# Kernel optimization log

Measured on AMD Instinct MI355X. Metric: run time of the kernel, lower is better.

The kernel has to match this reference:

```python
import jax, jax.numpy as jnp
import numpy as np
import math

B, S, E, H, F = 2, 2048, 1024, 16, 4096
D = E // H
EPS = 1e-5


def _layernorm(x, g, b):
    mu = jnp.mean(x, axis=-1, keepdims=True)
    var = jnp.mean(jnp.square(x - mu), axis=-1, keepdims=True)
    return (x - mu) * jax.lax.rsqrt(var + EPS) * g + b


def _xavier(k, fan_in, fan_out):
    limit = math.sqrt(6.0 / (fan_in + fan_out))
    return jax.random.uniform(k, (fan_in, fan_out), jnp.float32, -limit, limit)


def setup_inputs() -> dict:
    key = jax.random.key(0)
    ks = jax.random.split(key, 8)
    x = jax.random.normal(ks[0], (B, S, E), jnp.float32)
    # causal mask: 1 where attendable, 0 where masked (masked_fill at mask==0)
    mask = jnp.tril(jnp.ones((S, S), jnp.int32))[None, None]  # [1,1,S,S]
    return {
        "x": x,
        "mask": mask,
        "Wq": _xavier(ks[1], E, E), "bq": jnp.zeros((E,), jnp.float32),
        "Wk": _xavier(ks[2], E, E), "bk": jnp.zeros((E,), jnp.float32),
        "Wv": _xavier(ks[3], E, E), "bv": jnp.zeros((E,), jnp.float32),
        "Wo": _xavier(ks[4], E, E), "bo": jnp.zeros((E,), jnp.float32),
        "W1": _xavier(ks[5], E, F), "b1": jnp.zeros((F,), jnp.float32),
        "W2": _xavier(ks[6], F, E), "b2": jnp.zeros((E,), jnp.float32),
        "ln1_g": jnp.ones((E,), jnp.float32), "ln1_b": jnp.zeros((E,), jnp.float32),
        "ln2_g": jnp.ones((E,), jnp.float32), "ln2_b": jnp.zeros((E,), jnp.float32),
    }


def reference(x, mask, Wq, bq, Wk, bk, Wv, bv, Wo, bo, W1, b1, W2, b2,
              ln1_g, ln1_b, ln2_g, ln2_b):
    n = _layernorm(x, ln1_g, ln1_b)
    # project and split heads: [B,S,E] -> [B,H,S,D]
    def heads(w, b):
        return (n @ w + b).reshape(B, S, H, D).transpose(0, 2, 1, 3)
    Q, K, V = heads(Wq, bq), heads(Wk, bk), heads(Wv, bv)
    scores = jnp.einsum('bhsd,bhtd->bhst', Q, K) / math.sqrt(D)  # [B,H,S,S]
    scores = jnp.where(mask == 0, jnp.float32(-1e9), scores)
    attn = jax.nn.softmax(scores, axis=-1)
    ctx = jnp.einsum('bhst,bhtd->bhsd', attn, V)
    ctx = ctx.transpose(0, 2, 1, 3).reshape(B, S, E)
    attn_out = ctx @ Wo + bo
    x = _layernorm(x + attn_out, ln2_g, ln2_b)
    ffn = jax.nn.gelu(x @ W1 + b1, approximate=False) @ W2 + b2
    return x + ffn
```

## Files before the change

### kernel.cpp

```cpp
#include <hip/hip_runtime.h>
#include <cmath>

typedef unsigned short u16;
typedef unsigned int u32;
typedef __bf16 bf16x8 __attribute__((ext_vector_type(8)));
typedef float f32x4 __attribute__((ext_vector_type(4)));

#define SEQ 2048
#define EMB 1024
#define NHEAD 16
#define HDIM 64
#define FFDIM 4096
#define NBATCH 2
#define QKVLD 3072
#define PWS 68

#define QSCALE 0.18033688011112042f

__device__ __forceinline__ u16 f2bf(float f) {
  u32 u = __float_as_uint(f);
  u32 r = u + 0x7fffu + ((u >> 16) & 1u);
  return (u16)(r >> 16);
}

__device__ __forceinline__ float ex2(float x) {
#if __has_builtin(__builtin_amdgcn_exp2f)
  return __builtin_amdgcn_exp2f(x);
#else
  return exp2f(x);
#endif
}

__device__ __forceinline__ float geluf(float x) {
  float u = 0.7978845608028654f * (x + 0.044715f * x * x * x);
  float e = ex2(2.8853900817779268f * u);
  return x - x / (e + 1.0f);
}

__device__ __forceinline__ void gload16(const void* g, void* l) {
  __builtin_amdgcn_global_load_lds(
      (const __attribute__((address_space(1))) unsigned int*)g,
      (__attribute__((address_space(3))) unsigned int*)l, 16, 0, 0);
}

__global__ __launch_bounds__(256)
void wtrans_kernel(const float* __restrict__ W, u16* __restrict__ WT, int K, int N) {
  __shared__ float tile[32][33];
  int tx = threadIdx.x & 31, ty = threadIdx.x >> 5;
  int n0 = blockIdx.x * 32, k0 = blockIdx.y * 32;
#pragma unroll
  for (int i = 0; i < 32; i += 8)
    tile[ty + i][tx] = W[(size_t)(k0 + ty + i) * N + (n0 + tx)];
  __syncthreads();
#pragma unroll
  for (int i = 0; i < 32; i += 8)
    WT[(size_t)(n0 + ty + i) * K + (k0 + tx)] = f2bf(tile[tx][ty + i]);
}

__global__ __launch_bounds__(256)
void wtrans4_kernel(const float* __restrict__ W0, const float* __restrict__ W1_,
                    const float* __restrict__ W2_, const float* __restrict__ W3,
                    u16* __restrict__ Dqkv, u16* __restrict__ Do) {
  __shared__ float tile[32][33];
  int z = blockIdx.z;
  const float* W = (z == 0) ? W0 : (z == 1) ? W1_ : (z == 2) ? W2_ : W3;
  u16* D = (z < 3) ? (Dqkv + (size_t)z * EMB * EMB) : Do;
  int tx = threadIdx.x & 31, ty = threadIdx.x >> 5;
  int n0 = blockIdx.x * 32, k0 = blockIdx.y * 32;
#pragma unroll
  for (int i = 0; i < 32; i += 8)
    tile[ty + i][tx] = W[(size_t)(k0 + ty + i) * EMB + (n0 + tx)];
  __syncthreads();
#pragma unroll
  for (int i = 0; i < 32; i += 8)
    D[(size_t)(n0 + ty + i) * EMB + (k0 + tx)] = f2bf(tile[tx][ty + i]);
}

__global__ __launch_bounds__(256)
void vtrans_kernel(const u16* __restrict__ QKV, u16* __restrict__ Vt) {
  __shared__ u16 tile[64 * 72];
  int bh = blockIdx.y, b = bh >> 4, h = bh & 15;
  int s0 = blockIdx.x * 64;
  const u16* src = QKV + (size_t)b * SEQ * QKVLD + 2048 + (size_t)h * HDIM;
  int tid = threadIdx.x;
#pragma unroll
  for (int cc = 0; cc < 2; ++cc) {
    int c = tid + cc * 256;
    int s = c >> 3, d0 = (c & 7) * 8;
    uint4 v = *(const uint4*)(src + (size_t)(s0 + s) * QKVLD + d0);
    *(uint4*)(&tile[s * 72 + d0]) = v;
  }
  __syncthreads();
  u16* dst = Vt + (size_t)bh * HDIM * SEQ;
#pragma unroll
  for (int cc = 0; cc < 2; ++cc) {
    int c = tid + cc * 256;
    int d = c >> 3, t0l = (c & 7) * 8;
    union { uint4 u; u16 s[8]; } ou;
#pragma unroll
    for (int j = 0; j < 8; ++j) ou.s[j] = tile[(t0l + j) * 72 + d];
    *(uint4*)(dst + (size_t)d * SEQ + s0 + t0l) = ou.u;
  }
}

__global__ __launch_bounds__(256)
void ln_kernel(const float* __restrict__ in, const float* __restrict__ gamma,
               const float* __restrict__ beta, u16* __restrict__ outb) {
  int w = threadIdx.x >> 6, lane = threadIdx.x & 63;
  int row = blockIdx.x * 4 + w;
  size_t base = (size_t)row * EMB;
  float4 v[4];
  float s = 0.f, q = 0.f;
#pragma unroll
  for (int j = 0; j < 4; ++j) {
    v[j] = *(const float4*)(in + base + j * 256 + lane * 4);
    s += v[j].x + v[j].y + v[j].z + v[j].w;
    q += v[j].x * v[j].x + v[j].y * v[j].y + v[j].z * v[j].z + v[j].w * v[j].w;
  }
#pragma unroll
  for (int off = 1; off < 64; off <<= 1) {
    s += __shfl_xor(s, off);
    q += __shfl_xor(q, off);
  }
  float mean = s * (1.0f / EMB);
  float var = q * (1.0f / EMB) - mean * mean;
  float rstd = rsqrtf(var + 1e-5f);
#pragma unroll
  for (int j = 0; j < 4; ++j) {
    int c = j * 256 + lane * 4;
    float4 g4 = *(const float4*)(gamma + c);
    float4 b4 = *(const float4*)(beta + c);
    ushort4 ob;
    ob.x = f2bf((v[j].x - mean) * rstd * g4.x + b4.x);
    ob.y = f2bf((v[j].y - mean) * rstd * g4.y + b4.y);
    ob.z = f2bf((v[j].z - mean) * rstd * g4.z + b4.z);
    ob.w = f2bf((v[j].w - mean) * rstd * g4.w + b4.w);
    *(ushort4*)(outb + base + c) = ob;
  }
}

__global__ __launch_bounds__(256)
void ln2f_kernel(const float* __restrict__ p, size_t pstride,
                 const float* __restrict__ bias, const float* __restrict__ resid,
                 const float* __restrict__ gamma, const float* __restrict__ beta,
                 u16* __restrict__ outb, float* __restrict__ outf) {
  int w = threadIdx.x >> 6, lane = threadIdx.x & 63;
  int row = blockIdx.x * 4 + w;
  size_t base = (size_t)row * EMB;
  float4 v[4];
  float s = 0.f, q = 0.f;
#pragma unroll
  for (int j = 0; j < 4; ++j) {
    int c = j * 256 + lane * 4;
    float4 a = *(const float4*)(p + base + c);
    float4 b = *(const float4*)(p + pstride + base + c);
    float4 r = *(const float4*)(resid + base + c);
    float4 bb = *(const float4*)(bias + c);
    v[j].x = a.x + b.x + r.x + bb.x;
    v[j].y = a.y + b.y + r.y + bb.y;
    v[j].z = a.z + b.z + r.z + bb.z;
    v[j].w = a.w + b.w + r.w + bb.w;
    s += v[j].x + v[j].y + v[j].z + v[j].w;
    q += v[j].x * v[j].x + v[j].y * v[j].y + v[j].z * v[j].z + v[j].w * v[j].w;
  }
#pragma unroll
  for (int off = 1; off < 64; off <<= 1) {
    s += __shfl_xor(s, off);
    q += __shfl_xor(q, off);
  }
  float mean = s * (1.0f / EMB);
  float var = q * (1.0f / EMB) - mean * mean;
  float rstd = rsqrtf(var + 1e-5f);
#pragma unroll
  for (int j = 0; j < 4; ++j) {
    int c = j * 256 + lane * 4;
    float4 g4 = *(const float4*)(gamma + c);
    float4 b4 = *(const float4*)(beta + c);
    float y0 = (v[j].x - mean) * rstd * g4.x + b4.x;
    float y1 = (v[j].y - mean) * rstd * g4.y + b4.y;
    float y2 = (v[j].z - mean) * rstd * g4.z + b4.z;
    float y3 = (v[j].w - mean) * rstd * g4.w + b4.w;
    ushort4 ob;
    ob.x = f2bf(y0); ob.y = f2bf(y1); ob.z = f2bf(y2); ob.w = f2bf(y3);
    *(ushort4*)(outb + base + c) = ob;
    *(float4*)(outf + base + c) = make_float4(y0, y1, y2, y3);
  }
}

__global__ __launch_bounds__(256)
void reduce2_kernel(const float* __restrict__ p, size_t pstride,
                    const float* __restrict__ bias, const float* __restrict__ resid,
                    float* __restrict__ out, int ncols) {
  size_t i = ((size_t)blockIdx.x * 256 + threadIdx.x) * 4;
  float4 a = *(const float4*)(p + i);
  float4 b = *(const float4*)(p + pstride + i);
  float4 r = *(const float4*)(resid + i);
  int col = (int)(i & (size_t)(ncols - 1));
  float4 bb = *(const float4*)(bias + col);
  float4 o;
  o.x = a.x + b.x + r.x + bb.x;
  o.y = a.y + b.y + r.y + bb.y;
  o.z = a.z + b.z + r.z + bb.z;
  o.w = a.w + b.w + r.w + bb.w;
  *(float4*)(out + i) = o;
}

__global__ __launch_bounds__(256)
void gemm_bt(const u16* __restrict__ A, const u16* __restrict__ BT,
             const float* __restrict__ bias, const float* __restrict__ bias2,
             const float* __restrict__ bias3, void* __restrict__ out,
             const float* __restrict__ resid, int M, int N, int K,
             int mode, float scale, int ksplit,
             float* __restrict__ partial, size_t pstride) {
  __shared__ __align__(16) u16 As[128 * 64];
  __shared__ __align__(16) u16 Bs[128 * 64];
  int tid = threadIdx.x;
  int lane = tid & 63, w = tid >> 6;
  int wm = w >> 1, wn = w & 1;
  int g = lane >> 4, lr = lane & 15;
  int m0 = blockIdx.y * 128, n0 = blockIdx.x * 128;
  int z = blockIdx.z;
  int kbeg = z * ksplit, kend = kbeg + ksplit;

  f32x4 acc[4][4];
#pragma unroll
  for (int mt = 0; mt < 4; ++mt)
#pragma unroll
    for (int nt = 0; nt < 4; ++nt) {
      acc[mt][nt][0] = 0.f; acc[mt][nt][1] = 0.f;
      acc[mt][nt][2] = 0.f; acc[mt][nt][3] = 0.f;
    }

  size_t ao[4], bo_[4];
  int lo[4];
#pragma unroll
  for (int cc = 0; cc < 4; ++cc) {
    int c = tid + cc * 256;
    int row = c >> 3, slot = c & 7;
    int gc = slot ^ (row & 7);
    ao[cc] = (size_t)(m0 + row) * K + gc * 8;
    bo_[cc] = (size_t)(n0 + row) * K + gc * 8;
    lo[cc] = c * 8;
  }
  int swz[2];
#pragma unroll
  for (int kk = 0; kk < 2; ++kk) swz[kk] = ((kk * 4 + g) ^ (lr & 7)) * 8;

  for (int k0 = kbeg; k0 < kend; k0 += 64) {
    __syncthreads();
#pragma unroll
    for (int cc = 0; cc < 4; ++cc) gload16(A + ao[cc] + k0, As + lo[cc]);
#pragma unroll
    for (int cc = 0; cc < 4; ++cc) gload16(BT + bo_[cc] + k0, Bs + lo[cc]);
    __syncthreads();
#pragma unroll
    for (int kk = 0; kk < 2; ++kk) {
      bf16x8 af[4], bfr[4];
#pragma unroll
      for (int mt = 0; mt < 4; ++mt)
        af[mt] = *(const bf16x8*)(As + (wm * 64 + mt * 16 + lr) * 64 + swz[kk]);
#pragma unroll
      for (int nt = 0; nt < 4; ++nt)
        bfr[nt] = *(const bf16x8*)(Bs + (wn * 64 + nt * 16 + lr) * 64 + swz[kk]);
#pragma unroll
      for (int mt = 0; mt < 4; ++mt)
#pragma unroll
        for (int nt = 0; nt < 4; ++nt)
          acc[mt][nt] = __builtin_amdgcn_mfma_f32_16x16x32_bf16(af[mt], bfr[nt], acc[mt][nt], 0, 0, 0);
    }
  }

  float* pz = partial + (size_t)z * pstride;
#pragma unroll
  for (int mt = 0; mt < 4; ++mt) {
    int row = m0 + wm * 64 + mt * 16 + g * 4;
#pragma unroll
    for (int nt = 0; nt < 4; ++nt) {
      int col = n0 + wn * 64 + nt * 16 + lr;
      float bcol;
      if (mode == 3) {
        int which = col >> 10;
        const float* bp = (which == 0) ? bias : (which == 1) ? bias2 : bias3;
        bcol = bp[col & 1023];
      } else if (mode != 4) {
        bcol = bias[col];
      } else {
        bcol = 0.f;
      }
#pragma unroll
      for (int r = 0; r < 4; ++r) {
        float vacc = acc[mt][nt][r] + bcol;
        size_t idx = (size_t)(row + r) * N + col;
        if (mode == 0)      ((u16*)out)[idx] = f2bf(vacc * scale);
        else if (mode == 1) ((u16*)out)[idx] = f2bf(geluf(vacc));
        else if (mode == 2) ((float*)out)[idx] = vacc + resid[idx];
        else if (mode == 3) ((u16*)out)[idx] = f2bf(col < 1024 ? vacc * QSCALE : vacc);
        else                pz[idx] = vacc;
      }
    }
  }
}

__shared__ __align__(16) u16 attn_Kt[64 * 64];
__shared__ __align__(16) u16 attn_VT[64 * 64];
__shared__ __align__(16) u16 attn_Pw[2][4][16 * PWS];

template <int S0>
__device__ __forceinline__ void attn_tile(
    int t0, const int* q0, int w, int g, int lr, const bf16x8& ones,
    bf16x8 (&qf)[2][2], f32x4 (&lacc)[2], f32x4 (&oacc)[2][4]) {
  f32x4 sacc[2][4];
#pragma unroll
  for (int s = S0; s < 2; ++s)
#pragma unroll
    for (int nt = 0; nt < 4; ++nt) {
      sacc[s][nt][0] = 0.f; sacc[s][nt][1] = 0.f;
      sacc[s][nt][2] = 0.f; sacc[s][nt][3] = 0.f;
    }
#pragma unroll
  for (int kk = 0; kk < 2; ++kk)
#pragma unroll
    for (int nt = 0; nt < 4; ++nt) {
      int sw = ((kk * 4 + g) ^ lr) & 7;
      bf16x8 bfr = *(const bf16x8*)(&attn_Kt[(nt * 16 + lr) * 64 + sw * 8]);
      if (S0 == 0)
        sacc[0][nt] = __builtin_amdgcn_mfma_f32_16x16x32_bf16(qf[0][kk], bfr, sacc[0][nt], 0, 0, 0);
      sacc[1][nt] = __builtin_amdgcn_mfma_f32_16x16x32_bf16(qf[1][kk], bfr, sacc[1][nt], 0, 0, 0);
    }

#pragma unroll
  for (int s = S0; s < 2; ++s) {
    bool diag = (t0 == q0[s]);
#pragma unroll
    for (int r = 0; r < 4; ++r) {
#pragma unroll
      for (int nt = 0; nt < 4; ++nt) {
        float pv = ex2(sacc[s][nt][r]);
        if (diag && (nt * 16 + lr > w * 16 + g * 4 + r)) pv = 0.f;
        attn_Pw[s][w][(g * 4 + r) * PWS + nt * 16 + lr] = f2bf(pv);
      }
    }
  }

#pragma unroll
  for (int kk = 0; kk < 2; ++kk) {
    bf16x8 pf0, pf1;
    if (S0 == 0) pf0 = *(const bf16x8*)(&attn_Pw[0][w][lr * PWS + kk * 32 + g * 8]);
    pf1 = *(const bf16x8*)(&attn_Pw[1][w][lr * PWS + kk * 32 + g * 8]);
#pragma unroll
    for (int nt = 0; nt < 4; ++nt) {
      int sw = ((kk * 4 + g) ^ lr) & 7;
      bf16x8 vf = *(const bf16x8*)(&attn_VT[(nt * 16 + lr) * 64 + sw * 8]);
      if (S0 == 0)
        oacc[0][nt] = __builtin_amdgcn_mfma_f32_16x16x32_bf16(pf0, vf, oacc[0][nt], 0, 0, 0);
      oacc[1][nt] = __builtin_amdgcn_mfma_f32_16x16x32_bf16(pf1, vf, oacc[1][nt], 0, 0, 0);
    }
    if (S0 == 0)
      lacc[0] = __builtin_amdgcn_mfma_f32_16x16x32_bf16(pf0, ones, lacc[0], 0, 0, 0);
    lacc[1] = __builtin_amdgcn_mfma_f32_16x16x32_bf16(pf1, ones, lacc[1], 0, 0, 0);
  }
}

__global__ __launch_bounds__(256)
void attn2_kernel(const u16* __restrict__ QKV, const u16* __restrict__ Vt,
                  u16* __restrict__ ctx) {
  int tid = threadIdx.x, lane = tid & 63, w = tid >> 6;
  int g = lane >> 4, lr = lane & 15;
  int bh = blockIdx.y, b = bh >> 4, h = bh & 15;
  int q0[2];
  q0[0] = blockIdx.x * 64;
  q0[1] = (SEQ / 64 - 1 - blockIdx.x) * 64;
  const u16* Qh = QKV + (size_t)b * SEQ * QKVLD + (size_t)h * HDIM;
  const u16* Kh = Qh + 1024;
  const u16* Vth = Vt + (size_t)bh * HDIM * SEQ;

  bf16x8 ones;
#pragma unroll
  for (int j = 0; j < 8; ++j) ones[j] = (__bf16)1.0f;

  bf16x8 qf[2][2];
#pragma unroll
  for (int s = 0; s < 2; ++s)
#pragma unroll
    for (int kk = 0; kk < 2; ++kk)
      qf[s][kk] = *(const bf16x8*)(Qh + (size_t)(q0[s] + w * 16 + lr) * QKVLD + kk * 32 + g * 8);

  f32x4 lacc[2];
  f32x4 oacc[2][4];
#pragma unroll
  for (int s = 0; s < 2; ++s) {
    lacc[s][0] = 0.f; lacc[s][1] = 0.f; lacc[s][2] = 0.f; lacc[s][3] = 0.f;
#pragma unroll
    for (int nt = 0; nt < 4; ++nt) {
      oacc[s][nt][0] = 0.f; oacc[s][nt][1] = 0.f;
      oacc[s][nt][2] = 0.f; oacc[s][nt][3] = 0.f;
    }
  }

  int c1 = tid, c2 = tid + 256;
  int t1 = c1 >> 3, ch1 = (c1 ^ t1) & 7;
  int t2 = c2 >> 3, ch2 = (c2 ^ t2) & 7;
  for (int t0 = 0; t0 <= q0[1]; t0 += 64) {
    __syncthreads();
    gload16(Kh + (size_t)(t0 + t1) * QKVLD + ch1 * 8, attn_Kt + c1 * 8);
    gload16(Kh + (size_t)(t0 + t2) * QKVLD + ch2 * 8, attn_Kt + c2 * 8);
    gload16(Vth + (size_t)t1 * SEQ + t0 + ch1 * 8, attn_VT + c1 * 8);
    gload16(Vth + (size_t)t2 * SEQ + t0 + ch2 * 8, attn_VT + c2 * 8);
    __syncthreads();

    if (t0 <= q0[0])
      attn_tile<0>(t0, q0, w, g, lr, ones, qf, lacc, oacc);
    else
      attn_tile<1>(t0, q0, w, g, lr, ones, qf, lacc, oacc);
  }

#pragma unroll
  for (int s = 0; s < 2; ++s) {
    int srow = q0[s] + w * 16 + g * 4;
    float inv[4];
#pragma unroll
    for (int r = 0; r < 4; ++r) inv[r] = 1.0f / lacc[s][r];
#pragma unroll
    for (int nt = 0; nt < 4; ++nt) {
      int col = h * HDIM + nt * 16 + lr;
#pragma unroll
      for (int r = 0; r < 4; ++r) {
        float o = oacc[s][nt][r] * inv[r];
        ctx[((size_t)b * SEQ + srow + r) * EMB + col] = f2bf(o);
      }
    }
  }
}

extern "C" void kernel_launch(void* const* d_in, const int* in_sizes, int n_in,
                              void* d_out, int out_size, void* d_ws, size_t ws_size,
                              hipStream_t stream) {
  const float* x    = (const float*)d_in[0];
  const float* Wq   = (const float*)d_in[2];
  const float* bq   = (const float*)d_in[3];
  const float* Wk   = (const float*)d_in[4];
  const float* bk   = (const float*)d_in[5];
  const float* Wv   = (const float*)d_in[6];
  const float* bv   = (const float*)d_in[7];
  const float* Wo   = (const float*)d_in[8];
  const float* bo   = (const float*)d_in[9];
  const float* W1   = (const float*)d_in[10];
  const float* b1   = (const float*)d_in[11];
  const float* W2   = (const float*)d_in[12];
  const float* b2   = (const float*)d_in[13];
  const float* ln1g = (const float*)d_in[14];
  const float* ln1b = (const float*)d_in[15];
  const float* ln2g = (const float*)d_in[16];
  const float* ln2b = (const float*)d_in[17];

  char* ws = (char*)d_ws;
  u16* WqkvT = (u16*)(ws + ((size_t)0 << 20));
  u16* WoT   = (u16*)(ws + ((size_t)6 << 20));
  u16* W1T   = (u16*)(ws + ((size_t)8 << 20));
  u16* W2T   = (u16*)(ws + ((size_t)16 << 20));
  u16* xb    = (u16*)(ws + ((size_t)24 << 20));
  u16* QKVb  = (u16*)(ws + ((size_t)32 << 20));
  u16* ctxb  = (u16*)(ws + ((size_t)56 << 20));
  float* x2f = (float*)(ws + ((size_t)48 << 20));
  u16* x2b   = xb;
  u16* VtG   = (u16*)(ws + ((size_t)64 << 20));
  float* pWo = (float*)(ws + ((size_t)64 << 20));
  u16* h1    = (u16*)(ws + ((size_t)64 << 20));
  float* pF2 = (float*)(ws + ((size_t)0 << 20));

  dim3 blk(256);
  const int M = NBATCH * SEQ;

  wtrans4_kernel<<<dim3(32, 32, 4), blk, 0, stream>>>(Wq, Wk, Wv, Wo, WqkvT, WoT);
  wtrans_kernel<<<dim3(128, 32), blk, 0, stream>>>(W1, W1T, EMB, FFDIM);
  wtrans_kernel<<<dim3(32, 128), blk, 0, stream>>>(W2, W2T, FFDIM, EMB);

  ln_kernel<<<M / 4, blk, 0, stream>>>(x, ln1g, ln1b, xb);

  gemm_bt<<<dim3(QKVLD / 128, M / 128), blk, 0, stream>>>(
      xb, WqkvT, bq, bk, bv, QKVb, nullptr, M, QKVLD, EMB, 3, 1.0f, EMB, nullptr, 0);

  vtrans_kernel<<<dim3(SEQ / 64, NBATCH * NHEAD), blk, 0, stream>>>(QKVb, VtG);

  attn2_kernel<<<dim3(SEQ / 128, NBATCH * NHEAD), blk, 0, stream>>>(QKVb, VtG, ctxb);

  gemm_bt<<<dim3(EMB / 128, M / 128, 2), blk, 0, stream>>>(
      ctxb, WoT, nullptr, nullptr, nullptr, nullptr, nullptr, M, EMB, EMB, 4, 1.0f,
      EMB / 2, pWo, (size_t)4 << 20);

  ln2f_kernel<<<M / 4, blk, 0, stream>>>(pWo, (size_t)4 << 20, bo, x, ln2g, ln2b,
                                         x2b, x2f);

  gemm_bt<<<dim3(FFDIM / 128, M / 128), blk, 0, stream>>>(
      x2b, W1T, b1, nullptr, nullptr, h1, nullptr, M, FFDIM, EMB, 1, 1.0f, EMB, nullptr, 0);

  gemm_bt<<<dim3(EMB / 128, M / 128, 2), blk, 0, stream>>>(
      h1, W2T, nullptr, nullptr, nullptr, nullptr, nullptr, M, EMB, FFDIM, 4, 1.0f,
      FFDIM / 2, pF2, (size_t)8 << 20);
  reduce2_kernel<<<M * EMB / 1024, blk, 0, stream>>>(pF2, (size_t)8 << 20, b2, x2f,
                                                     (float*)d_out, EMB);
}
```

Measured before the change: 418.8 us.

## Replace GEMM with 8-wave double-buffered pipelined kernel and larger tiles

Replaces the simple single-buffered 128x128 GEMM with a templated 512-thread kernel that uses 256-wide N tiles and BM of 128 or 256. Global-to-LDS loads for later k-steps are interleaved with the MFMA phases across four LDS buffers, using explicit s_barrier, vmcnt waits and setprio. The intent is to hide memory latency and raise MFMA utilisation. The cost is much more LDS per block, fewer blocks on the smaller GEMMs, and fragile hand-written wait counts.

```diff
diff --git a/kernel.cpp b/kernel.cpp
--- a/kernel.cpp
+++ b/kernel.cpp
@@ -205,75 +205,141 @@
   *(float4*)(out + i) = o;
 }
 
-__global__ __launch_bounds__(256)
-void gemm_bt(const u16* __restrict__ A, const u16* __restrict__ BT,
-             const float* __restrict__ bias, const float* __restrict__ bias2,
-             const float* __restrict__ bias3, void* __restrict__ out,
-             const float* __restrict__ resid, int M, int N, int K,
-             int mode, float scale, int ksplit,
-             float* __restrict__ partial, size_t pstride) {
-  __shared__ __align__(16) u16 As[128 * 64];
-  __shared__ __align__(16) u16 Bs[128 * 64];
+
+#define BARM asm volatile("s_barrier" ::: "memory")
+#define VMWS asm volatile("s_waitcnt vmcnt(%0)" ::"n"(4 + RA) : "memory")
+#define VMW0 asm volatile("s_waitcnt vmcnt(0)" ::: "memory")
+#define NOSTG ((void)0)
+#define NOWT ((void)0)
+
+#define STG_A(t, d, kh)                                                       \
+  { _Pragma("unroll")                                                         \
+    for (int j = 0; j < RA; ++j)                                              \
+      gload16(A + (size_t)sgA[j] + kbeg + (t) * 64 + (kh) * 32,               \
+              As + ((d) * 2 + (kh)) * ABUF + slA[j]); }
+
+#define STG_B(t, d, kh)                                                       \
+  { _Pragma("unroll")                                                         \
+    for (int j = 0; j < 2; ++j)                                               \
+      gload16(BT + (size_t)sgB[j] + kbeg + (t) * 64 + (kh) * 32,              \
+              Bs + ((d) * 2 + (kh)) * 8192 + slB[j]); }
+
+#define PHASE(d, kk, mh, STAGE, WAITC)                                        \
+  {                                                                           \
+    if ((mh) == 0) {                                                          \
+      _Pragma("unroll")                                                       \
+      for (int nt = 0; nt < 4; ++nt)                                          \
+        bfr[nt] = *(const bf16x8*)(Bs + ((d) * 2 + (kk)) * 8192 + boff +      \
+                                   nt * 512);                                 \
+    }                                                                         \
+    bf16x8 af[MT2];                                                           \
+    _Pragma("unroll")                                                         \
+    for (int mi = 0; mi < MT2; ++mi)                                          \
+      af[mi] = *(const bf16x8*)(As + ((d) * 2 + (kk)) * ABUF + aoff +         \
+                                ((mh) * MT2 + mi) * 512);                     \
+    STAGE;                                                                    \
+    BARM;                                                                     \
+    __builtin_amdgcn_sched_barrier(0);                                        \
+    __builtin_amdgcn_s_setprio(1);                                            \
+    _Pragma("unroll")                                                         \
+    for (int mi = 0; mi < MT2; ++mi)                                          \
+      _Pragma("unroll")                                                       \
+      for (int nt = 0; nt < 4; ++nt)                                          \
+        acc[(mh) * MT2 + mi][nt] = __builtin_amdgcn_mfma_f32_16x16x32_bf16(   \
+            af[mi], bfr[nt], acc[(mh) * MT2 + mi][nt], 0, 0, 0);              \
+    __builtin_amdgcn_s_setprio(0);                                            \
+    __builtin_amdgcn_sched_barrier(0);                                        \
+    WAITC;                                                                    \
+    BARM;                                                                     \
+  }
+
+template <int BM>
+__global__ __launch_bounds__(512, 2)
+void gemm8(const u16* __restrict__ A, const u16* __restrict__ BT,
+           const float* __restrict__ bias, const float* __restrict__ bias2,
+           const float* __restrict__ bias3, void* __restrict__ out,
+           const float* __restrict__ resid, int M, int N, int K,
+           int mode, float scale, int ksplit,
+           float* __restrict__ partial, size_t pstride) {
+  constexpr int MT = BM / 32;
+  constexpr int MT2 = MT / 2;
+  constexpr int RA = BM / 128;
+  constexpr int ABUF = BM * 32;
+  __shared__ __align__(16) u16 As[4 * ABUF];
+  __shared__ __align__(16) u16 Bs[4 * 8192];
+
   int tid = threadIdx.x;
   int lane = tid & 63, w = tid >> 6;
-  int wm = w >> 1, wn = w & 1;
+  int wm = w >> 2, wn = w & 3;
   int g = lane >> 4, lr = lane & 15;
-  int m0 = blockIdx.y * 128, n0 = blockIdx.x * 128;
+  int m0 = blockIdx.y * BM, n0 = blockIdx.x * 256;
   int z = blockIdx.z;
-  int kbeg = z * ksplit, kend = kbeg + ksplit;
-
-  f32x4 acc[4][4];
-#pragma unroll
-  for (int mt = 0; mt < 4; ++mt)
+  size_t kbeg = (size_t)z * ksplit;
+  int nk = ksplit >> 6, npair = nk >> 1;
+
+  int phys = ((lr & 1) * 4 + g) ^ ((lr >> 1) & 7);
+  int aoff = wm * (BM / 2) * 32 + (lr >> 1) * 64 + phys * 8;
+  int boff = wn * 2048 + (lr >> 1) * 64 + phys * 8;
+
+  int sgA[RA], slA[RA];
+#pragma unroll
+  for (int j = 0; j < RA; ++j) {
+    int c = tid + j * 512;
+    int sr = c >> 3, ph = c & 7, l = ph ^ (sr & 7);
+    sgA[j] = (m0 + 2 * sr + (l >> 2)) * K + (l & 3) * 8;
+    slA[j] = c * 8;
+  }
+  int sgB[2], slB[2];
+#pragma unroll
+  for (int j = 0; j < 2; ++j) {
+    int c = tid + j * 512;
+    int sr = c >> 3, ph = c & 7, l = ph ^ (sr & 7);
+    sgB[j] = (n0 + 2 * sr + (l >> 2)) * K + (l & 3) * 8;
+    slB[j] = c * 8;
+  }
+
+  f32x4 acc[MT][4];
+#pragma unroll
+  for (int mt = 0; mt < MT; ++mt)
 #pragma unroll
     for (int nt = 0; nt < 4; ++nt) {
       acc[mt][nt][0] = 0.f; acc[mt][nt][1] = 0.f;
       acc[mt][nt][2] = 0.f; acc[mt][nt][3] = 0.f;
     }
 
-  size_t ao[4], bo_[4];
-  int lo[4];
-#pragma unroll
-  for (int cc = 0; cc < 4; ++cc) {
-    int c = tid + cc * 256;
-    int row = c >> 3, slot = c & 7;
-    int gc = slot ^ (row & 7);
-    ao[cc] = (size_t)(m0 + row) * K + gc * 8;
-    bo_[cc] = (size_t)(n0 + row) * K + gc * 8;
-    lo[cc] = c * 8;
-  }
-  int swz[2];
-#pragma unroll
-  for (int kk = 0; kk < 2; ++kk) swz[kk] = ((kk * 4 + g) ^ (lr & 7)) * 8;
-
-  for (int k0 = kbeg; k0 < kend; k0 += 64) {
-    __syncthreads();
-#pragma unroll
-    for (int cc = 0; cc < 4; ++cc) gload16(A + ao[cc] + k0, As + lo[cc]);
-#pragma unroll
-    for (int cc = 0; cc < 4; ++cc) gload16(BT + bo_[cc] + k0, Bs + lo[cc]);
-    __syncthreads();
-#pragma unroll
-    for (int kk = 0; kk < 2; ++kk) {
-      bf16x8 af[4], bfr[4];
-#pragma unroll
-      for (int mt = 0; mt < 4; ++mt)
-        af[mt] = *(const bf16x8*)(As + (wm * 64 + mt * 16 + lr) * 64 + swz[kk]);
-#pragma unroll
-      for (int nt = 0; nt < 4; ++nt)
-        bfr[nt] = *(const bf16x8*)(Bs + (wn * 64 + nt * 16 + lr) * 64 + swz[kk]);
-#pragma unroll
-      for (int mt = 0; mt < 4; ++mt)
-#pragma unroll
-        for (int nt = 0; nt < 4; ++nt)
-          acc[mt][nt] = __builtin_amdgcn_mfma_f32_16x16x32_bf16(af[mt], bfr[nt], acc[mt][nt], 0, 0, 0);
-    }
+  bf16x8 bfr[4];
+
+  STG_B(0, 0, 0); STG_A(0, 0, 0); STG_B(0, 0, 1); STG_A(0, 0, 1);
+  STG_B(1, 1, 0); STG_A(1, 1, 0); STG_B(1, 1, 1);
+  VMWS; BARM;
+
+  for (int it = 0; it < npair - 1; ++it) {
+    int t1 = 2 * it + 1, t2 = 2 * it + 2, t3 = 2 * it + 3;
+    PHASE(0, 0, 0, STG_A(t1, 1, 1), NOWT)
+    PHASE(0, 0, 1, STG_B(t2, 0, 0), NOWT)
+    PHASE(0, 1, 0, STG_A(t2, 0, 0), NOWT)
+    PHASE(0, 1, 1, STG_B(t2, 0, 1), VMWS)
+    PHASE(1, 0, 0, STG_A(t2, 0, 1), NOWT)
+    PHASE(1, 0, 1, STG_B(t3, 1, 0), NOWT)
+    PHASE(1, 1, 0, STG_A(t3, 1, 0), NOWT)
+    PHASE(1, 1, 1, STG_B(t3, 1, 1), VMWS)
+  }
+  {
+    int t1 = nk - 1;
+    PHASE(0, 0, 0, STG_A(t1, 1, 1), NOWT)
+    PHASE(0, 0, 1, NOSTG, NOWT)
+    PHASE(0, 1, 0, NOSTG, NOWT)
+    PHASE(0, 1, 1, NOSTG, VMW0)
+    PHASE(1, 0, 0, NOSTG, NOWT)
+    PHASE(1, 0, 1, NOSTG, NOWT)
+    PHASE(1, 1, 0, NOSTG, NOWT)
+    PHASE(1, 1, 1, NOSTG, NOWT)
   }
 
   float* pz = partial + (size_t)z * pstride;
 #pragma unroll
-  for (int mt = 0; mt < 4; ++mt) {
-    int row = m0 + wm * 64 + mt * 16 + g * 4;
+  for (int mt = 0; mt < MT; ++mt) {
+    int row = m0 + wm * (BM / 2) + mt * 16 + g * 4;
 #pragma unroll
     for (int nt = 0; nt < 4; ++nt) {
       int col = n0 + wn * 64 + nt * 16 + lr;
@@ -469,6 +535,7 @@
   float* pF2 = (float*)(ws + ((size_t)0 << 20));
 
   dim3 blk(256);
+  dim3 blk512(512);
   const int M = NBATCH * SEQ;
 
   wtrans4_kernel<<<dim3(32, 32, 4), blk, 0, stream>>>(Wq, Wk, Wv, Wo, WqkvT, WoT);
@@ -477,24 +544,25 @@
 
   ln_kernel<<<M / 4, blk, 0, stream>>>(x, ln1g, ln1b, xb);
 
-  gemm_bt<<<dim3(QKVLD / 128, M / 128), blk, 0, stream>>>(
+  gemm8<256><<<dim3(QKVLD / 256, M / 256), blk512, 0, stream>>>(
       xb, WqkvT, bq, bk, bv, QKVb, nullptr, M, QKVLD, EMB, 3, 1.0f, EMB, nullptr, 0);
 
   vtrans_kernel<<<dim3(SEQ / 64, NBATCH * NHEAD), blk, 0, stream>>>(QKVb, VtG);
 
   attn2_kernel<<<dim3(SEQ / 128, NBATCH * NHEAD), blk, 0, stream>>>(QKVb, VtG, ctxb);
 
-  gemm_bt<<<dim3(EMB / 128, M / 128, 2), blk, 0, stream>>>(
+  gemm8<128><<<dim3(EMB / 256, M / 128, 2), blk512, 0, stream>>>(
       ctxb, WoT, nullptr, nullptr, nullptr, nullptr, nullptr, M, EMB, EMB, 4, 1.0f,
       EMB / 2, pWo, (size_t)4 << 20);
 
   ln2f_kernel<<<M / 4, blk, 0, stream>>>(pWo, (size_t)4 << 20, bo, x, ln2g, ln2b,
                                          x2b, x2f);
 
-  gemm_bt<<<dim3(FFDIM / 128, M / 128), blk, 0, stream>>>(
-      x2b, W1T, b1, nullptr, nullptr, h1, nullptr, M, FFDIM, EMB, 1, 1.0f, EMB, nullptr, 0);
-
-  gemm_bt<<<dim3(EMB / 128, M / 128, 2), blk, 0, stream>>>(
+  gemm8<256><<<dim3(FFDIM / 256, M / 256), blk512, 0, stream>>>(
+      x2b, W1T, b1, nullptr, nullptr, h1, nullptr, M, FFDIM, EMB, 1, 1.0f, EMB,
+      nullptr, 0);
+
+  gemm8<128><<<dim3(EMB / 256, M / 128, 2), blk512, 0, stream>>>(
       h1, W2T, nullptr, nullptr, nullptr, nullptr, nullptr, M, EMB, FFDIM, 4, 1.0f,
       FFDIM / 2, pF2, (size_t)8 << 20);
   reduce2_kernel<<<M * EMB / 1024, blk, 0, stream>>>(pF2, (size_t)8 << 20, b2, x2f,
```

Result: slower. 428.8 us (+2.4%).

## Add software-pipelined double-buffered GEMM with XCD tile swizzle for Wo and FFN

Applied to the files above, without the earlier changes.

Adds a new GEMM kernel, gemm8n, used for the Wo projection and both FFN GEMMs. It double-buffers K-halves in LDS, interleaves async global-to-LDS loads with MFMA phases, uses swizzled inline ds_read_b128 addressing, raises wave priority during MFMA and allows two blocks per CU. It also remaps block indices so each XCD works on a spatially clustered group of tiles, aiming for better L2 reuse, and applies a simpler XCD swizzle to the existing gemm_bt. The cost targeted is load latency and barrier stalls in the GEMMs. In exchange the code is complex, relies on hand-placed waitcnts and assumes the grid size divides evenly by 8.

```diff
diff --git a/kernel.cpp b/kernel.cpp
--- a/kernel.cpp
+++ b/kernel.cpp
@@ -41,6 +41,40 @@
   __builtin_amdgcn_global_load_lds(
       (const __attribute__((address_space(1))) unsigned int*)g,
       (__attribute__((address_space(3))) unsigned int*)l, 16, 0, 0);
+}
+
+__device__ __forceinline__ u32 lds_addr(const void* p) {
+  return (u32)(size_t)(const __attribute__((address_space(3))) void*)p;
+}
+
+template <int IMM>
+__device__ __forceinline__ bf16x8 dsr16(u32 a) {
+  bf16x8 r;
+  asm volatile("ds_read_b128 %0, %1 offset:%2" : "=v"(r) : "v"(a), "n"(IMM));
+  return r;
+}
+
+__device__ __forceinline__ void xcd_swizzle(int gx, int gy, int& bx, int& by) {
+  int nwg = gx * gy;
+  int lin = blockIdx.x + gx * blockIdx.y;
+  int q = nwg >> 3;
+  int nl = (lin & 7) * q + (lin >> 3);
+  bx = nl % gx;
+  by = nl / gx;
+}
+
+template <int TX>
+__device__ __forceinline__ void xcd_tile_swizzle(int gx, int gy, int& bx, int& by) {
+  int nwg = gx * gy;
+  int lin = blockIdx.x + gx * blockIdx.y;
+  int c = lin & 7;
+  int wdx = lin >> 3;
+  int q = nwg >> 3;
+  int TY = q / TX;
+  int ncx = gx / TX;
+  int xt = c % ncx, yt = c / ncx;
+  bx = xt * TX + wdx % TX;
+  by = yt * TY + wdx / TX;
 }
 
 __global__ __launch_bounds__(256)
@@ -218,7 +252,9 @@
   int lane = tid & 63, w = tid >> 6;
   int wm = w >> 1, wn = w & 1;
   int g = lane >> 4, lr = lane & 15;
-  int m0 = blockIdx.y * 128, n0 = blockIdx.x * 128;
+  int bx, by;
+  xcd_swizzle(gridDim.x, gridDim.y, bx, by);
+  int m0 = by * 128, n0 = bx * 128;
   int z = blockIdx.z;
   int kbeg = z * ksplit, kend = kbeg + ksplit;
 
@@ -268,6 +304,161 @@
         for (int nt = 0; nt < 4; ++nt)
           acc[mt][nt] = __builtin_amdgcn_mfma_f32_16x16x32_bf16(af[mt], bfr[nt], acc[mt][nt], 0, 0, 0);
     }
+  }
+
+  float* pz = partial + (size_t)z * pstride;
+#pragma unroll
+  for (int mt = 0; mt < 4; ++mt) {
+    int row = m0 + wm * 64 + mt * 16 + g * 4;
+#pragma unroll
+    for (int nt = 0; nt < 4; ++nt) {
+      int col = n0 + wn * 64 + nt * 16 + lr;
+      float bcol;
+      if (mode == 3) {
+        int which = col >> 10;
+        const float* bp = (which == 0) ? bias : (which == 1) ? bias2 : bias3;
+        bcol = bp[col & 1023];
+      } else if (mode != 4) {
+        bcol = bias[col];
+      } else {
+        bcol = 0.f;
+      }
+#pragma unroll
+      for (int r = 0; r < 4; ++r) {
+        float vacc = acc[mt][nt][r] + bcol;
+        size_t idx = (size_t)(row + r) * N + col;
+        if (mode == 0)      ((u16*)out)[idx] = f2bf(vacc * scale);
+        else if (mode == 1) ((u16*)out)[idx] = f2bf(geluf(vacc));
+        else if (mode == 2) ((float*)out)[idx] = vacc + resid[idx];
+        else if (mode == 3) ((u16*)out)[idx] = f2bf(col < 1024 ? vacc * QSCALE : vacc);
+        else                pz[idx] = vacc;
+      }
+    }
+  }
+}
+
+
+#define BARM __builtin_amdgcn_s_barrier()
+#define VMW6 asm volatile("s_waitcnt vmcnt(6)")
+#define VMW0 asm volatile("s_waitcnt vmcnt(0)")
+#define NOSTG ((void)0)
+#define NOWT ((void)0)
+#define NABUF (128 * 32)
+
+#define STGN_A(t, d, kh)                                                      \
+  { gload16(A + (size_t)sgA[0] + kbeg + (t) * 64 + (kh) * 32,                 \
+            As + ((d) * 2 + (kh)) * NABUF + sl[0]);                           \
+    gload16(A + (size_t)sgA[1] + kbeg + (t) * 64 + (kh) * 32,                 \
+            As + ((d) * 2 + (kh)) * NABUF + sl[1]); }
+
+#define STGN_B(t, d, kh)                                                      \
+  { gload16(BT + (size_t)sgB[0] + kbeg + (t) * 64 + (kh) * 32,                \
+            Bs + ((d) * 2 + (kh)) * NABUF + sl[0]);                           \
+    gload16(BT + (size_t)sgB[1] + kbeg + (t) * 64 + (kh) * 32,                \
+            Bs + ((d) * 2 + (kh)) * NABUF + sl[1]); }
+
+#define PHASEN(d, kk, mh, STAGE, WAITC)                                       \
+  {                                                                           \
+    const u32 bA = bB + ((d) * 2 + (kk)) * (NABUF * 2);                       \
+    const u32 aA = aB + ((d) * 2 + (kk)) * (NABUF * 2);                       \
+    if ((mh) == 0) {                                                          \
+      bfr[0] = dsr16<0>(bA);                                                  \
+      bfr[1] = dsr16<1024>(bA);                                               \
+      bfr[2] = dsr16<2048>(bA);                                               \
+      bfr[3] = dsr16<3072>(bA);                                               \
+    }                                                                         \
+    bf16x8 af[2];                                                             \
+    af[0] = dsr16<(((mh) * 2 + 0) * 1024)>(aA);                               \
+    af[1] = dsr16<(((mh) * 2 + 1) * 1024)>(aA);                               \
+    STAGE;                                                                    \
+    BARM;                                                                     \
+    asm volatile("s_waitcnt lgkmcnt(0)");                                     \
+    __builtin_amdgcn_sched_barrier(0);                                        \
+    __builtin_amdgcn_s_setprio(1);                                            \
+    _Pragma("unroll")                                                         \
+    for (int mi = 0; mi < 2; ++mi)                                            \
+      _Pragma("unroll")                                                       \
+      for (int nt = 0; nt < 4; ++nt)                                          \
+        acc[(mh) * 2 + mi][nt] = __builtin_amdgcn_mfma_f32_16x16x32_bf16(     \
+            af[mi], bfr[nt], acc[(mh) * 2 + mi][nt], 0, 0, 0);                \
+    __builtin_amdgcn_s_setprio(0);                                            \
+    WAITC;                                                                    \
+    BARM;                                                                     \
+  }
+
+template <int TXS>
+__global__ __launch_bounds__(256, 2)
+void gemm8n(const u16* __restrict__ A, const u16* __restrict__ BT,
+            const float* __restrict__ bias, const float* __restrict__ bias2,
+            const float* __restrict__ bias3, void* __restrict__ out,
+            const float* __restrict__ resid, int M, int N, int K,
+            int mode, float scale, int ksplit,
+            float* __restrict__ partial, size_t pstride) {
+  __shared__ __align__(16) u16 As[4 * NABUF];
+  __shared__ __align__(16) u16 Bs[4 * NABUF];
+  int tid = threadIdx.x;
+  int lane = tid & 63, w = tid >> 6;
+  int wm = w >> 1, wn = w & 1;
+  int g = lane >> 4, lr = lane & 15;
+  int bx, by;
+  xcd_tile_swizzle<TXS>(gridDim.x, gridDim.y, bx, by);
+  int m0 = by * 128, n0 = bx * 128;
+  int z = blockIdx.z;
+  size_t kbeg = (size_t)z * ksplit;
+  int nk = ksplit >> 6, npair = nk >> 1;
+
+  int phys = ((lr & 1) * 4 + g) ^ ((lr >> 1) & 7);
+  int aoff = wm * 64 * 32 + (lr >> 1) * 64 + phys * 8;
+  int boff = wn * 64 * 32 + (lr >> 1) * 64 + phys * 8;
+  const u32 aB = lds_addr(As) + 2 * aoff;
+  const u32 bB = lds_addr(Bs) + 2 * boff;
+
+  int sgA[2], sgB[2], sl[2];
+#pragma unroll
+  for (int j = 0; j < 2; ++j) {
+    int c = tid + j * 256;
+    int sr = c >> 3, ph = c & 7, l = ph ^ (sr & 7);
+    sgA[j] = (m0 + 2 * sr + (l >> 2)) * K + (l & 3) * 8;
+    sgB[j] = (n0 + 2 * sr + (l >> 2)) * K + (l & 3) * 8;
+    sl[j] = c * 8;
+  }
+
+  f32x4 acc[4][4];
+#pragma unroll
+  for (int mt = 0; mt < 4; ++mt)
+#pragma unroll
+    for (int nt = 0; nt < 4; ++nt) {
+      acc[mt][nt][0] = 0.f; acc[mt][nt][1] = 0.f;
+      acc[mt][nt][2] = 0.f; acc[mt][nt][3] = 0.f;
+    }
+
+  bf16x8 bfr[4];
+
+  STGN_B(0, 0, 0); STGN_A(0, 0, 0); STGN_B(0, 0, 1); STGN_A(0, 0, 1);
+  STGN_B(1, 1, 0); STGN_A(1, 1, 0); STGN_B(1, 1, 1);
+  VMW6; BARM;
+
+  for (int it = 0; it < npair - 1; ++it) {
+    int t1 = 2 * it + 1, t2 = 2 * it + 2, t3 = 2 * it + 3;
+    PHASEN(0, 0, 0, STGN_A(t1, 1, 1), NOWT)
+    PHASEN(0, 0, 1, STGN_B(t2, 0, 0), NOWT)
+    PHASEN(0, 1, 0, STGN_A(t2, 0, 0), NOWT)
+    PHASEN(0, 1, 1, STGN_B(t2, 0, 1), VMW6)
+    PHASEN(1, 0, 0, STGN_A(t2, 0, 1), NOWT)
+    PHASEN(1, 0, 1, STGN_B(t3, 1, 0), NOWT)
+    PHASEN(1, 1, 0, STGN_A(t3, 1, 0), NOWT)
+    PHASEN(1, 1, 1, STGN_B(t3, 1, 1), VMW6)
+  }
+  {
+    int t1 = nk - 1;
+    PHASEN(0, 0, 0, STGN_A(t1, 1, 1), NOWT)
+    PHASEN(0, 0, 1, NOSTG, NOWT)
+    PHASEN(0, 1, 0, NOSTG, NOWT)
+    PHASEN(0, 1, 1, NOSTG, VMW0)
+    PHASEN(1, 0, 0, NOSTG, NOWT)
+    PHASEN(1, 0, 1, NOSTG, NOWT)
+    PHASEN(1, 1, 0, NOSTG, NOWT)
+    PHASEN(1, 1, 1, NOSTG, NOWT)
   }
 
   float* pz = partial + (size_t)z * pstride;
@@ -484,17 +675,18 @@
 
   attn2_kernel<<<dim3(SEQ / 128, NBATCH * NHEAD), blk, 0, stream>>>(QKVb, VtG, ctxb);
 
-  gemm_bt<<<dim3(EMB / 128, M / 128, 2), blk, 0, stream>>>(
+  gemm8n<4><<<dim3(EMB / 128, M / 128, 2), blk, 0, stream>>>(
       ctxb, WoT, nullptr, nullptr, nullptr, nullptr, nullptr, M, EMB, EMB, 4, 1.0f,
       EMB / 2, pWo, (size_t)4 << 20);
 
   ln2f_kernel<<<M / 4, blk, 0, stream>>>(pWo, (size_t)4 << 20, bo, x, ln2g, ln2b,
                                          x2b, x2f);
 
-  gemm_bt<<<dim3(FFDIM / 128, M / 128), blk, 0, stream>>>(
-      x2b, W1T, b1, nullptr, nullptr, h1, nullptr, M, FFDIM, EMB, 1, 1.0f, EMB, nullptr, 0);
-
-  gemm_bt<<<dim3(EMB / 128, M / 128, 2), blk, 0, stream>>>(
+  gemm8n<8><<<dim3(FFDIM / 128, M / 128), blk, 0, stream>>>(
+      x2b, W1T, b1, nullptr, nullptr, h1, nullptr, M, FFDIM, EMB, 1, 1.0f, EMB,
+      nullptr, 0);
+
+  gemm8n<4><<<dim3(EMB / 128, M / 128, 2), blk, 0, stream>>>(
       h1, W2T, nullptr, nullptr, nullptr, nullptr, nullptr, M, EMB, FFDIM, 4, 1.0f,
       FFDIM / 2, pF2, (size_t)8 << 20);
   reduce2_kernel<<<M * EMB / 1024, blk, 0, stream>>>(pF2, (size_t)8 << 20, b2, x2f,
```

After: 404.9 us. 3.3% less time.
